# Kernel tuning notes

Hardware: AMD Instinct MI355X
Metric: run time of the kernel (lower is better)

Reference implementation:

```python
import jax, jax.numpy as jnp
import numpy as np
import math
from math import factorial

MUL = 128            # channel multiplicity of in1 and out
LS = [0, 1, 2]       # l values of the three irreps in each input/output
N_PATH_W = MUL * 1 * MUL  # uvw weight block per path (mul2 == 1)

# ---- Wigner 3j (real basis), following e3nn's construction ----

def _su2_cg(j1, m1, j2, m2, j3, m3):
    if m3 != m1 + m2:
        return 0.0
    vmin = int(max(-j1 + j2 + m3, -j1 + m1, 0))
    vmax = int(min(j2 + j3 + m1, j3 - j1 + j2, j3 + m3))
    if vmax < vmin:
        return 0.0
    f = lambda n: factorial(int(round(n)))
    pref = (2 * j3 + 1) * (f(j3 + j1 - j2) * f(j3 - j1 + j2) * f(j1 + j2 - j3) * f(j3 + m3) * f(j3 - m3)) / (
        f(j1 + j2 + j3 + 1) * f(j1 - m1) * f(j1 + m1) * f(j2 - m2) * f(j2 + m2))
    S = 0.0
    for v in range(vmin, vmax + 1):
        S += (-1) ** (v + j2 + m2) * (f(j2 + j3 + m1 - v) * f(j1 - m1 + v)) / (
            f(v) * f(j3 - j1 + j2 - v) * f(j3 + m3 - v) * f(v + j1 - j2 - m3))
    return math.sqrt(pref) * S


def _q(l):
    # change of basis real -> complex spherical harmonics (e3nn convention)
    q = np.zeros((2 * l + 1, 2 * l + 1), dtype=np.complex128)
    for m in range(-l, 0):
        q[l + m, l + abs(m)] = 1 / math.sqrt(2)
        q[l + m, l - abs(m)] = -1j / math.sqrt(2)
    q[l, l] = 1
    for m in range(1, l + 1):
        q[l + m, l + abs(m)] = (-1) ** m / math.sqrt(2)
        q[l + m, l - abs(m)] = 1j * (-1) ** m / math.sqrt(2)
    return (-1j) ** l * q


def _w3j(l1, l2, l3):
    C = np.zeros((2 * l1 + 1, 2 * l2 + 1, 2 * l3 + 1))
    for m1 in range(-l1, l1 + 1):
        for m2 in range(-l2, l2 + 1):
            m3 = m1 + m2
            if abs(m3) <= l3:
                C[m1 + l1, m2 + l2, m3 + l3] = _su2_cg(l1, m1, l2, m2, l3, m3)
    Q1, Q2, Q3 = _q(l1), _q(l2), _q(l3)
    Cc = np.einsum('ij,kl,mn,ikn->jlm', Q1, Q2, np.conj(Q3.T), C.astype(np.complex128))
    Cr, Ci = Cc.real, Cc.imag
    Cp = Cr if np.linalg.norm(Cr) >= np.linalg.norm(Ci) else Ci
    return (Cp / np.linalg.norm(Cp)).astype(np.float32)

# allowed (l1, l2) -> l_out paths for 0e/1o/2e x 0e/1o/2e -> 0e/1o/2e
PATHS = [(0, 0, 0), (0, 1, 1), (0, 2, 2), (1, 0, 1), (1, 1, 0), (1, 1, 2),
         (1, 2, 1), (2, 0, 2), (2, 1, 1), (2, 2, 0), (2, 2, 2)]
# path_normalization='element': alpha = (2*l_out+1) / sum over paths to same out of mul1*mul2
_FAN = {o: sum(MUL for (_, _, c) in PATHS if c == o) for o in LS}
PW = {o: math.sqrt((2 * o + 1) / _FAN[o]) for o in LS}
W3J = {(a, b, c): _w3j(a, b, c) for (a, b, c) in PATHS}


def _split1(x):
    # [N, 1152] -> list of [N, 128, 2l+1]
    parts, off = [], 0
    for l in LS:
        d = MUL * (2 * l + 1)
        parts.append(x[:, off:off + d].reshape(-1, MUL, 2 * l + 1))
        off += d
    return parts


def _split2(x):
    # [N, 9] -> list of [N, 2l+1]
    parts, off = [], 0
    for l in LS:
        parts.append(x[:, off:off + 2 * l + 1])
        off += 2 * l + 1
    return parts


def _fctp(x1, x2, weight):
    xs1, xs2 = _split1(x1), _split2(x2)
    N = x1.shape[0]
    outs = [jnp.zeros((N, MUL, 2 * l + 1), x1.dtype) for l in LS]
    off = 0
    for (l1, l2, lo) in PATHS:
        w = weight[off:off + N_PATH_W].reshape(MUL, MUL)  # [u, w] (v == 1)
        off += N_PATH_W
        C = jnp.asarray(W3J[(l1, l2, lo)])  # [2l1+1, 2l2+1, 2lo+1]
        t = jnp.einsum('ijk,nui,nj->nuk', C, xs1[l1], xs2[l2])
        outs[lo] = outs[lo] + PW[lo] * jnp.einsum('uw,nuk->nwk', w, t)
    return jnp.concatenate([o.reshape(N, -1) for o in outs], axis=1)


def setup_inputs() -> dict:
    key = jax.random.key(0)
    k1, k2, k3 = jax.random.split(key, 3)
    N = 20000
    return {
        'x1': jax.random.normal(k1, (N, MUL * 9), dtype=jnp.float32),
        'x2': jax.random.normal(k2, (N, 9), dtype=jnp.float32),
        'weight': jax.random.normal(k3, (len(PATHS) * N_PATH_W,), dtype=jnp.float32),
    }


def reference(x1, x2, weight):
    return _fctp(x1, x2, weight)
```

## Files before the change

### kernel.cpp

```cpp
#include <hip/hip_runtime.h>
#include <math.h>

#define NPATH 11
#define SROW 1152
#define SAMP 16
#define NTHREADS 512

constexpr int H_L1[11]  = {0,0,0,1,1,1,1,2,2,2,2};
constexpr int H_L2[11]  = {0,1,2,0,1,1,2,0,1,2,2};
constexpr int H_LO[11]  = {0,1,2,1,0,2,1,2,1,0,2};
constexpr int H_N1[11]  = {1,1,1,3,3,3,3,5,5,5,5};
constexpr int H_N2[11]  = {1,3,5,1,3,3,5,1,3,5,5};
constexpr int H_N3[11]  = {1,3,5,3,1,5,3,5,3,1,5};
constexpr int H_PIB[12] = {0,1,2,3,6,9,12,15,20,25,30,35};
constexpr int H_MOFF[12]  = {0,1,4,9,18,21,36,45,70,85,90,115};
constexpr int H_W3OFF[12] = {0,1,10,35,44,53,98,143,168,213,238,363};
constexpr int H_X2OFF[3]  = {0,1,4};
constexpr int H_CBASE[3]  = {0,1,4};
constexpr int H_KCB[3]    = {0,1,4};
constexpr float H_PW[3] = {0.05103103630798288f, 0.07654655446197431f, 0.09882117688026186f};

namespace w3c {

constexpr double fact(int n) {
    double r = 1.0;
    for (int i = 2; i <= n; ++i) r *= (double)i;
    return r;
}

constexpr double csqrt(double x) {
    if (x <= 0.0) return 0.0;
    double g = x < 1.0 ? 1.0 : x;
    for (int i = 0; i < 100; ++i) g = 0.5 * (g + x / g);
    return g;
}

constexpr double su2_cg(int j1, int m1, int j2, int m2, int j3, int m3) {
    if (m3 != m1 + m2) return 0.0;
    int vmin = -j1 + j2 + m3;
    if (-j1 + m1 > vmin) vmin = -j1 + m1;
    if (0 > vmin) vmin = 0;
    int vmax = j2 + j3 + m1;
    if (j3 - j1 + j2 < vmax) vmax = j3 - j1 + j2;
    if (j3 + m3 < vmax) vmax = j3 + m3;
    if (vmax < vmin) return 0.0;
    double pref = (2.0 * j3 + 1.0) *
        (fact(j3 + j1 - j2) * fact(j3 - j1 + j2) * fact(j1 + j2 - j3) *
         fact(j3 + m3) * fact(j3 - m3)) /
        (fact(j1 + j2 + j3 + 1) * fact(j1 - m1) * fact(j1 + m1) *
         fact(j2 - m2) * fact(j2 + m2));
    double S = 0.0;
    for (int v = vmin; v <= vmax; ++v) {
        double sgn = ((v + j2 + m2) & 1) ? -1.0 : 1.0;
        S += sgn * (fact(j2 + j3 + m1 - v) * fact(j1 - m1 + v)) /
             (fact(v) * fact(j3 - j1 + j2 - v) * fact(j3 + m3 - v) *
              fact(v + j1 - j2 - m3));
    }
    return csqrt(pref) * S;
}

struct Q { double re[5][5]; double im[5][5]; };

constexpr Q build_q(int l) {
    Q q{};
    double s = csqrt(0.5);
    for (int m = -l; m < 0; ++m) {
        q.re[l + m][l - m] = s;
        q.im[l + m][l + m] = -s;
    }
    q.re[l][l] = 1.0;
    for (int m = 1; m <= l; ++m) {
        double sg = (m & 1) ? -1.0 : 1.0;
        q.re[l + m][l + m] = sg * s;
        q.im[l + m][l - m] = sg * s;
    }
    double fr = 1.0, fi = 0.0;
    if (l == 1) { fr = 0.0; fi = -1.0; }
    else if (l == 2) { fr = -1.0; fi = 0.0; }
    for (int r = 0; r < 5; ++r)
        for (int c = 0; c < 5; ++c) {
            double a = q.re[r][c], b = q.im[r][c];
            q.re[r][c] = a * fr - b * fi;
            q.im[r][c] = a * fi + b * fr;
        }
    return q;
}

struct PathW { float v[125]; };

constexpr PathW make_path(int l1, int l2, int l3) {
    int n1 = 2 * l1 + 1, n2 = 2 * l2 + 1, n3 = 2 * l3 + 1;
    double C[5][5][5] = {};
    for (int m1 = -l1; m1 <= l1; ++m1)
        for (int m2 = -l2; m2 <= l2; ++m2) {
            int m3 = m1 + m2;
            if (m3 >= -l3 && m3 <= l3)
                C[m1 + l1][m2 + l2][m3 + l3] = su2_cg(l1, m1, l2, m2, l3, m3);
        }
    Q q1 = build_q(l1), q2 = build_q(l2), q3 = build_q(l3);

    double Cr[5][5][5] = {}, Ci[5][5][5] = {};
    for (int j = 0; j < n1; ++j)
        for (int l = 0; l < n2; ++l)
            for (int m = 0; m < n3; ++m) {
                double ar = 0.0, ai = 0.0;
                for (int i = 0; i < n1; ++i)
                    for (int k = 0; k < n2; ++k) {
                        double t1r = q1.re[i][j], t1i = q1.im[i][j];
                        double t2r = q2.re[k][l], t2i = q2.im[k][l];
                        double tr = t1r * t2r - t1i * t2i;
                        double ti = t1r * t2i + t1i * t2r;
                        for (int n = 0; n < n3; ++n) {
                            double c = C[i][k][n];
                            if (c == 0.0) continue;
                            double pr = q3.re[n][m], pi = -q3.im[n][m];
                            ar += c * (tr * pr - ti * pi);
                            ai += c * (tr * pi + ti * pr);
                        }
                    }
                Cr[j][l][m] = ar;
                Ci[j][l][m] = ai;
            }

    double nr = 0.0, ni = 0.0;
    for (int j = 0; j < n1; ++j)
        for (int l = 0; l < n2; ++l)
            for (int m = 0; m < n3; ++m) {
                nr += Cr[j][l][m] * Cr[j][l][m];
                ni += Ci[j][l][m] * Ci[j][l][m];
            }
    nr = csqrt(nr);
    ni = csqrt(ni);
    bool useR = (nr >= ni);
    double norm = useR ? nr : ni;

    PathW out{};
    int idx = 0;
    for (int j = 0; j < n1; ++j)
        for (int l = 0; l < n2; ++l)
            for (int m = 0; m < n3; ++m)
                out.v[idx++] = (float)((useR ? Cr[j][l][m] : Ci[j][l][m]) / norm);
    return out;
}

constexpr PathW P0  = make_path(0,0,0);
constexpr PathW P1  = make_path(0,1,1);
constexpr PathW P2  = make_path(0,2,2);
constexpr PathW P3  = make_path(1,0,1);
constexpr PathW P4  = make_path(1,1,0);
constexpr PathW P5  = make_path(1,1,2);
constexpr PathW P6  = make_path(1,2,1);
constexpr PathW P7  = make_path(2,0,2);
constexpr PathW P8  = make_path(2,1,1);
constexpr PathW P9  = make_path(2,2,0);
constexpr PathW P10 = make_path(2,2,2);

struct W3All { float v[363]; };

constexpr W3All make_all() {
    W3All a{};
    const PathW* ps[11] = {&P0,&P1,&P2,&P3,&P4,&P5,&P6,&P7,&P8,&P9,&P10};
    for (int p = 0; p < 11; ++p) {
        int n = H_W3OFF[p+1] - H_W3OFF[p];
        for (int i = 0; i < n; ++i) a.v[H_W3OFF[p] + i] = ps[p]->v[i];
    }
    return a;
}

}

__device__ __constant__ w3c::W3All c_W3 = w3c::make_all();

typedef float f32x4 __attribute__((ext_vector_type(4)));
typedef __bf16 bf16x8 __attribute__((ext_vector_type(8)));

__device__ __forceinline__ unsigned short f2bf(float f) {
    union { float f; unsigned int u; } v; v.f = f;
    unsigned int u = v.u + 0x7fffu + ((v.u >> 16) & 1u);
    return (unsigned short)(u >> 16);
}

#define MFMA(a, b, c) __builtin_amdgcn_mfma_f32_16x16x32_bf16((a), (b), (c), 0, 0, 0)

__global__ __launch_bounds__(256) void wprep_kernel(
    const float* __restrict__ w, unsigned short* __restrict__ whi)
{
    int idx = blockIdx.x * 256 + threadIdx.x;
    if (idx >= NPATH * 128 * 128) return;
    int p   = idx / 16384;
    int rem = idx - p * 16384;
    int wc  = rem >> 7;
    int u   = rem & 127;
    whi[idx] = f2bf(w[p * 16384 + u * 128 + wc]);
}

template<int P0G, int NP, int CB, int NC>
__device__ __forceinline__ void gemm_pass(
    const unsigned short* __restrict__ whi,
    const unsigned short (*sB)[16][136],
    const float* sM35,
    float (&ov)[4][9], int r16, int q4, int wt)
{
    f32x4 acc[NP][NC];
    #pragma unroll
    for (int pp = 0; pp < NP; ++pp)
        #pragma unroll
        for (int i = 0; i < NC; ++i) acc[pp][i] = (f32x4)(0.0f);

    #pragma unroll
    for (int ub = 0; ub < 4; ++ub) {
        const int ko = ub * 32 + q4 * 8;
        bf16x8 B[NC];
        #pragma unroll
        for (int c = 0; c < NC; ++c)
            B[c] = *(const bf16x8*)&sB[CB + c][r16][ko];
        #pragma unroll
        for (int pp = 0; pp < NP; ++pp) {
            const size_t aoff =
                ((size_t)((P0G + pp) * 128 + wt * 16 + r16)) * 128 + ko;
            bf16x8 Ah = *(const bf16x8*)&whi[aoff];
            #pragma unroll
            for (int i = 0; i < NC; ++i)
                acc[pp][i] = MFMA(Ah, B[i], acc[pp][i]);
        }
    }

    #pragma unroll
    for (int pp = 0; pp < NP; ++pp) {
        const int P = P0G + pp;
        #pragma unroll
        for (int i = 0; i < NC; ++i)
            #pragma unroll
            for (int k = 0; k < H_N3[P]; ++k) {
                const float mv = sM35[r16 * 175 + (H_PIB[P] + i) * 5 + k];
                #pragma unroll
                for (int r = 0; r < 4; ++r)
                    ov[r][H_KCB[H_LO[P]] + k] += acc[pp][i][r] * mv;
            }
    }
}

__global__ __launch_bounds__(NTHREADS, 1) void fctp_kernel(
    const float* __restrict__ x1, const float* __restrict__ x2,
    const unsigned short* __restrict__ whi,
    float* __restrict__ out, int N)
{
    __shared__ __align__(16) unsigned char smem[50368];
    unsigned short (*sB)[16][136] = (unsigned short (*)[16][136])smem;
    float* sM35 = (float*)(smem + 39168);

    const int tid  = threadIdx.x;
    const int lane = tid & 63;
    const int wt   = tid >> 6;
    const int n0   = blockIdx.x * SAMP;

    {
        f32x4 tv[9];
        #pragma unroll
        for (int t = 0; t < 9; ++t) {
            const int e  = tid + t * NTHREADS;
            const int n  = e / 288;
            const int c4 = (e % 288) * 4;
            tv[t] = (n0 + n < N) ? *(const f32x4*)&x1[(size_t)(n0 + n) * SROW + c4]
                                 : (f32x4)(0.0f);
        }
        #pragma unroll
        for (int t = 0; t < 9; ++t) {
            const int e  = tid + t * NTHREADS;
            const int n  = e / 288;
            const int c4 = (e % 288) * 4;
            #pragma unroll
            for (int j = 0; j < 4; ++j) {
                int c = c4 + j;
                int col, u;
                if (c < 128)       { col = 0;           u = c; }
                else if (c < 512)  { int rr = c - 128;  u = rr / 3; col = 1 + rr % 3; }
                else               { int rr = c - 512;  u = rr / 5; col = 4 + rr % 5; }
                sB[col][n][u] = f2bf(tv[t][j]);
            }
        }
    }

    for (int e = tid; e < SAMP * 115; e += NTHREADS) {
        int n = e / 115, m = e % 115;
        float val = 0.0f;
        int pi5 = 0;
        #pragma unroll
        for (int p = 0; p < NPATH; ++p) {
            if (m >= H_MOFF[p] && m < H_MOFF[p + 1]) {
                const int n2 = H_N2[p], n3 = H_N3[p];
                int rr = m - H_MOFF[p];
                int i = rr / n3, k = rr % n3;
                if (n0 + n < N) {
                    const float* Cp  = c_W3.v + H_W3OFF[p];
                    const float* x2p = x2 + (size_t)(n0 + n) * 9 + H_X2OFF[H_L2[p]];
                    float a = 0.0f;
                    #pragma unroll
                    for (int j = 0; j < n2; ++j)
                        a += Cp[(i * n2 + j) * n3 + k] * x2p[j];
                    val = H_PW[H_LO[p]] * a;
                }
                pi5 = (H_PIB[p] + i) * 5 + k;
            }
        }
        sM35[n * 175 + pi5] = val;
    }
    __syncthreads();

    const int r16 = lane & 15;
    const int q4  = lane >> 4;

    float ov[4][9];
    #pragma unroll
    for (int r = 0; r < 4; ++r)
        #pragma unroll
        for (int j = 0; j < 9; ++j) ov[r][j] = 0.0f;

    gemm_pass<0, 3, 0, 1>(whi, sB, sM35, ov, r16, q4, wt);
    gemm_pass<3, 2, 1, 3>(whi, sB, sM35, ov, r16, q4, wt);
    gemm_pass<5, 2, 1, 3>(whi, sB, sM35, ov, r16, q4, wt);
    gemm_pass<7, 2, 4, 5>(whi, sB, sM35, ov, r16, q4, wt);
    gemm_pass<9, 2, 4, 5>(whi, sB, sM35, ov, r16, q4, wt);

    __syncthreads();
    float* sOut = (float*)smem;
    const int wbase = wt * 16 + q4 * 4;
    #pragma unroll
    for (int half = 0; half < 2; ++half) {
        if ((r16 >> 3) == half) {
            const int nl = r16 & 7;
            float* so = &sOut[nl * 1156];
            #pragma unroll
            for (int r = 0; r < 4; ++r) {
                const int w = wbase + r;
                so[w] = ov[r][0];
                #pragma unroll
                for (int k = 0; k < 3; ++k) so[128 + w * 3 + k] = ov[r][1 + k];
                #pragma unroll
                for (int k = 0; k < 5; ++k) so[512 + w * 5 + k] = ov[r][4 + k];
            }
        }
        __syncthreads();
        for (int e = tid; e < 8 * (SROW / 4); e += NTHREADS) {
            int nn = e / (SROW / 4), c4 = (e % (SROW / 4)) * 4;
            int n = half * 8 + nn;
            if (n0 + n < N)
                *(f32x4*)&out[(size_t)(n0 + n) * SROW + c4] =
                    *(const f32x4*)&sOut[nn * 1156 + c4];
        }
        __syncthreads();
    }
}

extern "C" void kernel_launch(void* const* d_in, const int* in_sizes, int n_in,
                              void* d_out, int out_size, void* d_ws, size_t ws_size,
                              hipStream_t stream) {
    const float* x1 = (const float*)d_in[0];
    const float* x2 = (const float*)d_in[1];
    const float* wt = (const float*)d_in[2];
    float* out = (float*)d_out;

    unsigned short* whi = (unsigned short*)d_ws;

    int N = in_sizes[0] / SROW;

    hipLaunchKernelGGL(wprep_kernel, dim3((NPATH * 128 * 128 + 255) / 256),
                       dim3(256), 0, stream, wt, whi);

    int blocks = (N + SAMP - 1) / SAMP;
    hipLaunchKernelGGL(fctp_kernel, dim3(blocks), dim3(NTHREADS), 0, stream,
                       x1, x2, whi, out, N);
}
```

Measured before the change: 131.1 us.

## Make blocks persistent over several tiles and prefetch next tile's x1 during GEMM

Each block now handles TPB=5 consecutive 16-sample tiles instead of one. It issues global loads for the next tile's x1 into registers before the MFMA passes, then writes them to shared memory after a barrier. The output staging buffer is moved to its own shared region so all 16 rows go out in one pass, and the l=2 GEMM passes are split to one path each. Block count drops about fivefold (roughly 250 blocks, close to the CU count), which risks load imbalance and the larger shared footprint. The extra prefetch registers may also raise register pressure.

```diff
diff --git a/kernel.cpp b/kernel.cpp
--- a/kernel.cpp
+++ b/kernel.cpp
@@ -5,6 +5,7 @@
 #define SROW 1152
 #define SAMP 16
 #define NTHREADS 512
+#define TPB 5
 
 constexpr int H_L1[11]  = {0,0,0,1,1,1,1,2,2,2,2};
 constexpr int H_L2[11]  = {0,1,2,0,1,1,2,0,1,2,2};
@@ -194,93 +195,42 @@
     whi[idx] = f2bf(w[p * 16384 + u * 128 + wc]);
 }
 
-template<int P0G, int NP, int CB, int NC>
-__device__ __forceinline__ void gemm_pass(
-    const unsigned short* __restrict__ whi,
-    const unsigned short (*sB)[16][136],
-    const float* sM35,
-    float (&ov)[4][9], int r16, int q4, int wt)
-{
-    f32x4 acc[NP][NC];
+__device__ __forceinline__ void issue_loads(
+    const float* __restrict__ x1, int n0, int N, f32x4 (&tv)[9], int tid)
+{
     #pragma unroll
-    for (int pp = 0; pp < NP; ++pp)
-        #pragma unroll
-        for (int i = 0; i < NC; ++i) acc[pp][i] = (f32x4)(0.0f);
-
+    for (int t = 0; t < 9; ++t) {
+        const int e  = tid + t * NTHREADS;
+        const int n  = e / 288;
+        const int c4 = (e % 288) * 4;
+        tv[t] = (n0 + n < N) ? *(const f32x4*)&x1[(size_t)(n0 + n) * SROW + c4]
+                             : (f32x4)(0.0f);
+    }
+}
+
+__device__ __forceinline__ void stage_write(
+    const f32x4 (&tv)[9], unsigned short (*sB)[16][136], int tid)
+{
     #pragma unroll
-    for (int ub = 0; ub < 4; ++ub) {
-        const int ko = ub * 32 + q4 * 8;
-        bf16x8 B[NC];
-        #pragma unroll
-        for (int c = 0; c < NC; ++c)
-            B[c] = *(const bf16x8*)&sB[CB + c][r16][ko];
-        #pragma unroll
-        for (int pp = 0; pp < NP; ++pp) {
-            const size_t aoff =
-                ((size_t)((P0G + pp) * 128 + wt * 16 + r16)) * 128 + ko;
-            bf16x8 Ah = *(const bf16x8*)&whi[aoff];
-            #pragma unroll
-            for (int i = 0; i < NC; ++i)
-                acc[pp][i] = MFMA(Ah, B[i], acc[pp][i]);
-        }
-    }
-
-    #pragma unroll
-    for (int pp = 0; pp < NP; ++pp) {
-        const int P = P0G + pp;
-        #pragma unroll
-        for (int i = 0; i < NC; ++i)
-            #pragma unroll
-            for (int k = 0; k < H_N3[P]; ++k) {
-                const float mv = sM35[r16 * 175 + (H_PIB[P] + i) * 5 + k];
-                #pragma unroll
-                for (int r = 0; r < 4; ++r)
-                    ov[r][H_KCB[H_LO[P]] + k] += acc[pp][i][r] * mv;
-            }
-    }
-}
-
-__global__ __launch_bounds__(NTHREADS, 1) void fctp_kernel(
-    const float* __restrict__ x1, const float* __restrict__ x2,
-    const unsigned short* __restrict__ whi,
-    float* __restrict__ out, int N)
-{
-    __shared__ __align__(16) unsigned char smem[50368];
-    unsigned short (*sB)[16][136] = (unsigned short (*)[16][136])smem;
-    float* sM35 = (float*)(smem + 39168);
-
-    const int tid  = threadIdx.x;
-    const int lane = tid & 63;
-    const int wt   = tid >> 6;
-    const int n0   = blockIdx.x * SAMP;
-
-    {
-        f32x4 tv[9];
-        #pragma unroll
-        for (int t = 0; t < 9; ++t) {
-            const int e  = tid + t * NTHREADS;
-            const int n  = e / 288;
-            const int c4 = (e % 288) * 4;
-            tv[t] = (n0 + n < N) ? *(const f32x4*)&x1[(size_t)(n0 + n) * SROW + c4]
-                                 : (f32x4)(0.0f);
-        }
-        #pragma unroll
-        for (int t = 0; t < 9; ++t) {
-            const int e  = tid + t * NTHREADS;
-            const int n  = e / 288;
-            const int c4 = (e % 288) * 4;
-            #pragma unroll
-            for (int j = 0; j < 4; ++j) {
-                int c = c4 + j;
-                int col, u;
-                if (c < 128)       { col = 0;           u = c; }
-                else if (c < 512)  { int rr = c - 128;  u = rr / 3; col = 1 + rr % 3; }
-                else               { int rr = c - 512;  u = rr / 5; col = 4 + rr % 5; }
-                sB[col][n][u] = f2bf(tv[t][j]);
-            }
-        }
-    }
-
+    for (int t = 0; t < 9; ++t) {
+        const int e  = tid + t * NTHREADS;
+        const int n  = e / 288;
+        const int c4 = (e % 288) * 4;
+        #pragma unroll
+        for (int j = 0; j < 4; ++j) {
+            int c = c4 + j;
+            int col, u;
+            if (c < 128)       { col = 0;           u = c; }
+            else if (c < 512)  { int rr = c - 128;  u = rr / 3; col = 1 + rr % 3; }
+            else               { int rr = c - 512;  u = rr / 5; col = 4 + rr % 5; }
+            sB[col][n][u] = f2bf(tv[t][j]);
+        }
+    }
+}
+
+__device__ __forceinline__ void stage_m35(
+    const float* __restrict__ x2, int n0, int N, float* sM35, int tid)
+{
     for (int e = tid; e < SAMP * 115; e += NTHREADS) {
         int n = e / 115, m = e % 115;
         float val = 0.0f;
@@ -305,50 +255,132 @@
         }
         sM35[n * 175 + pi5] = val;
     }
+}
+
+template<int P0G, int NP, int CB, int NC>
+__device__ __forceinline__ void gemm_pass(
+    const unsigned short* __restrict__ whi,
+    const unsigned short (*sB)[16][136],
+    const float* sM35,
+    float (&ov)[4][9], int r16, int q4, int wt)
+{
+    f32x4 acc[NP][NC];
+    #pragma unroll
+    for (int pp = 0; pp < NP; ++pp)
+        #pragma unroll
+        for (int i = 0; i < NC; ++i) acc[pp][i] = (f32x4)(0.0f);
+
+    #pragma unroll
+    for (int ub = 0; ub < 4; ++ub) {
+        const int ko = ub * 32 + q4 * 8;
+        bf16x8 B[NC];
+        #pragma unroll
+        for (int c = 0; c < NC; ++c)
+            B[c] = *(const bf16x8*)&sB[CB + c][r16][ko];
+        #pragma unroll
+        for (int pp = 0; pp < NP; ++pp) {
+            const size_t aoff =
+                ((size_t)((P0G + pp) * 128 + wt * 16 + r16)) * 128 + ko;
+            bf16x8 Ah = *(const bf16x8*)&whi[aoff];
+            #pragma unroll
+            for (int i = 0; i < NC; ++i)
+                acc[pp][i] = MFMA(Ah, B[i], acc[pp][i]);
+        }
+    }
+
+    #pragma unroll
+    for (int pp = 0; pp < NP; ++pp) {
+        const int P = P0G + pp;
+        #pragma unroll
+        for (int i = 0; i < NC; ++i)
+            #pragma unroll
+            for (int k = 0; k < H_N3[P]; ++k) {
+                const float mv = sM35[r16 * 175 + (H_PIB[P] + i) * 5 + k];
+                #pragma unroll
+                for (int r = 0; r < 4; ++r)
+                    ov[r][H_KCB[H_LO[P]] + k] += acc[pp][i][r] * mv;
+            }
+    }
+}
+
+__global__ __launch_bounds__(NTHREADS, 1) void fctp_kernel(
+    const float* __restrict__ x1, const float* __restrict__ x2,
+    const unsigned short* __restrict__ whi,
+    float* __restrict__ out, int N, int ntiles)
+{
+    __shared__ __align__(16) unsigned char smem[124352];
+    unsigned short (*sB)[16][136] = (unsigned short (*)[16][136])smem;
+    float* sM35 = (float*)(smem + 39168);
+    float* sOut = (float*)(smem + 50368);
+
+    const int tid  = threadIdx.x;
+    const int lane = tid & 63;
+    const int wt   = tid >> 6;
+    const int r16  = lane & 15;
+    const int q4   = lane >> 4;
+
+    const int t0 = blockIdx.x * TPB;
+    const int K  = (ntiles - t0 < TPB) ? (ntiles - t0) : TPB;
+    if (K <= 0) return;
+
+    f32x4 tv[9];
+
+    issue_loads(x1, t0 * SAMP, N, tv, tid);
+    stage_m35(x2, t0 * SAMP, N, sM35, tid);
+    stage_write(tv, sB, tid);
     __syncthreads();
 
-    const int r16 = lane & 15;
-    const int q4  = lane >> 4;
-
-    float ov[4][9];
-    #pragma unroll
-    for (int r = 0; r < 4; ++r)
-        #pragma unroll
-        for (int j = 0; j < 9; ++j) ov[r][j] = 0.0f;
-
-    gemm_pass<0, 3, 0, 1>(whi, sB, sM35, ov, r16, q4, wt);
-    gemm_pass<3, 2, 1, 3>(whi, sB, sM35, ov, r16, q4, wt);
-    gemm_pass<5, 2, 1, 3>(whi, sB, sM35, ov, r16, q4, wt);
-    gemm_pass<7, 2, 4, 5>(whi, sB, sM35, ov, r16, q4, wt);
-    gemm_pass<9, 2, 4, 5>(whi, sB, sM35, ov, r16, q4, wt);
-
-    __syncthreads();
-    float* sOut = (float*)smem;
-    const int wbase = wt * 16 + q4 * 4;
-    #pragma unroll
-    for (int half = 0; half < 2; ++half) {
-        if ((r16 >> 3) == half) {
-            const int nl = r16 & 7;
-            float* so = &sOut[nl * 1156];
+    for (int k = 0; k < K; ++k) {
+        const int n0 = (t0 + k) * SAMP;
+        const bool more = (k + 1 < K);
+
+        if (more) issue_loads(x1, n0 + SAMP, N, tv, tid);
+
+        float ov[4][9];
+        #pragma unroll
+        for (int r = 0; r < 4; ++r)
+            #pragma unroll
+            for (int j = 0; j < 9; ++j) ov[r][j] = 0.0f;
+
+        gemm_pass<0, 3, 0, 1>(whi, sB, sM35, ov, r16, q4, wt);
+        gemm_pass<3, 2, 1, 3>(whi, sB, sM35, ov, r16, q4, wt);
+        gemm_pass<5, 2, 1, 3>(whi, sB, sM35, ov, r16, q4, wt);
+        gemm_pass<7, 1, 4, 5>(whi, sB, sM35, ov, r16, q4, wt);
+        gemm_pass<8, 1, 4, 5>(whi, sB, sM35, ov, r16, q4, wt);
+        gemm_pass<9, 1, 4, 5>(whi, sB, sM35, ov, r16, q4, wt);
+        gemm_pass<10, 1, 4, 5>(whi, sB, sM35, ov, r16, q4, wt);
+
+        __syncthreads();
+
+        if (more) {
+            stage_write(tv, sB, tid);
+            stage_m35(x2, n0 + SAMP, N, sM35, tid);
+        }
+        {
+            const int wbase = wt * 16 + q4 * 4;
+            float* so = &sOut[r16 * 1156];
             #pragma unroll
             for (int r = 0; r < 4; ++r) {
                 const int w = wbase + r;
                 so[w] = ov[r][0];
                 #pragma unroll
-                for (int k = 0; k < 3; ++k) so[128 + w * 3 + k] = ov[r][1 + k];
+                for (int kk = 0; kk < 3; ++kk) so[128 + w * 3 + kk] = ov[r][1 + kk];
                 #pragma unroll
-                for (int k = 0; k < 5; ++k) so[512 + w * 5 + k] = ov[r][4 + k];
+                for (int kk = 0; kk < 5; ++kk) so[512 + w * 5 + kk] = ov[r][4 + kk];
             }
         }
         __syncthreads();
-        for (int e = tid; e < 8 * (SROW / 4); e += NTHREADS) {
-            int nn = e / (SROW / 4), c4 = (e % (SROW / 4)) * 4;
-            int n = half * 8 + nn;
-            if (n0 + n < N)
-                *(f32x4*)&out[(size_t)(n0 + n) * SROW + c4] =
+
+        #pragma unroll
+        for (int t = 0; t < 9; ++t) {
+            const int e  = tid + t * NTHREADS;
+            const int nn = e / 288;
+            const int c4 = (e % 288) * 4;
+            const int gn = n0 + nn;
+            if (gn < N)
+                *(f32x4*)&out[(size_t)gn * SROW + c4] =
                     *(const f32x4*)&sOut[nn * 1156 + c4];
         }
-        __syncthreads();
     }
 }
 
@@ -363,11 +395,12 @@
     unsigned short* whi = (unsigned short*)d_ws;
 
     int N = in_sizes[0] / SROW;
+    int ntiles = (N + SAMP - 1) / SAMP;
 
     hipLaunchKernelGGL(wprep_kernel, dim3((NPATH * 128 * 128 + 255) / 256),
                        dim3(256), 0, stream, wt, whi);
 
-    int blocks = (N + SAMP - 1) / SAMP;
+    int blocks = (ntiles + TPB - 1) / TPB;
     hipLaunchKernelGGL(fctp_kernel, dim3(blocks), dim3(NTHREADS), 0, stream,
-                       x1, x2, whi, out, N);
-}
+                       x1, x2, whi, out, N, ntiles);
+}
```

New measurement: 459.0 us. +250.1%, slower.
